# Kernel tuning notes

Measured on AMD Instinct MI355X. Metric: run time of the kernel, lower is better.

The kernel has to match this reference:

```python
import jax, jax.numpy as jnp
import numpy as np

B, HW, ENC, E, D, A, V, L = 64, 14, 2048, 512, 512, 512, 32000, 32
LN_EPS = 1e-5


def setup_inputs() -> dict:
    key = jax.random.key(0)
    ks = jax.random.split(key, 16)
    s = 0.02
    n = lambda k, sh: jax.random.normal(k, sh, jnp.float32)
    encoder_out = n(ks[0], (B, HW, HW, ENC))
    encoded_captions = jax.random.randint(ks[1], (B, L), 0, V)
    caption_lengths = jax.random.randint(ks[2], (B, 1), 2, L + 1)
    caption_lengths = caption_lengths.at[0, 0].set(L)  # ensure max length present
    return dict(
        encoder_out=encoder_out,
        encoded_captions=encoded_captions,
        caption_lengths=caption_lengths,
        emb=n(ks[3], (V, E)) * s,
        W_enc_att=n(ks[4], (A, ENC)) * s, b_enc_att=jnp.zeros((A,)),
        W_dec_att=n(ks[5], (A, D)) * s, b_dec_att=jnp.zeros((A,)),
        W_full_att=n(ks[6], (1, A)) * s, b_full_att=jnp.zeros((1,)),
        W_ih=n(ks[7], (4 * D, E + ENC)) * s, b_ih=jnp.zeros((4 * D,)),
        W_hh=n(ks[8], (4 * D, D)) * s, b_hh=jnp.zeros((4 * D,)),
        g_h=jnp.ones((D,)), be_h=jnp.zeros((D,)),
        g_c=jnp.ones((D,)), be_c=jnp.zeros((D,)),
        W_init_h=n(ks[9], (D, ENC)) * s, b_init_h=jnp.zeros((D,)),
        W_init_c=n(ks[10], (D, ENC)) * s, b_init_c=jnp.zeros((D,)),
        W_beta=n(ks[11], (ENC, D)) * s, b_beta=jnp.zeros((ENC,)),
        W_fc=n(ks[12], (V, D)) * s, b_fc=jnp.zeros((V,)),
    )


def _layer_norm(x, g, b):
    m = x.mean(-1, keepdims=True)
    v = ((x - m) ** 2).mean(-1, keepdims=True)
    return (x - m) / jnp.sqrt(v + LN_EPS) * g + b


def reference(encoder_out, encoded_captions, caption_lengths, emb,
              W_enc_att, b_enc_att, W_dec_att, b_dec_att, W_full_att, b_full_att,
              W_ih, b_ih, W_hh, b_hh, g_h, be_h, g_c, be_c,
              W_init_h, b_init_h, W_init_c, b_init_c, W_beta, b_beta, W_fc, b_fc):
    bsz = encoder_out.shape[0]
    enc_out = encoder_out.reshape(bsz, -1, encoder_out.shape[-1])  # [B,P,ENC]
    lengths = caption_lengths[:, 0]
    order = jnp.argsort(-lengths)  # stable descending sort (matches torch sort)
    lengths = lengths[order]
    enc_out = enc_out[order]
    caps = encoded_captions[order]
    embeds = emb[caps]  # [B,L,E]
    decode_lengths = lengths - 1
    T = caps.shape[1] - 1  # static max(decode_lengths)

    mean_enc = enc_out.mean(axis=1)
    h = _layer_norm(mean_enc @ W_init_h.T + b_init_h, g_h, be_h)
    c = _layer_norm(mean_enc @ W_init_c.T + b_init_c, g_c, be_c)

    att1 = enc_out @ W_enc_att.T + b_enc_att  # [B,P,A] precomputed once
    prev_seq = jnp.swapaxes(embeds[:, :T], 0, 1)  # [T,B,E] teacher-forced inputs
    masks = jnp.arange(T)[:, None] < decode_lengths[None, :]  # [T,B] active rows

    def step(carry, xs):
        h, c = carry
        prev, mask = xs
        # attention
        att2 = h @ W_dec_att.T + b_dec_att  # [B,A]
        e = jax.nn.relu(att1 + att2[:, None, :]) @ W_full_att[0] + b_full_att[0]  # [B,P]
        alpha = jax.nn.softmax(e, axis=1)
        awe = jnp.einsum('bpe,bp->be', enc_out, alpha)  # [B,ENC]
        gate = jax.nn.sigmoid(h @ W_beta.T + b_beta)
        awe = gate * awe
        # LSTM cell
        x = jnp.concatenate([prev, awe], axis=1)  # [B,E+ENC]
        gates = x @ W_ih.T + b_ih + h @ W_hh.T + b_hh
        i, f, g, o = jnp.split(gates, 4, axis=1)
        c_new = jax.nn.sigmoid(f) * c + jax.nn.sigmoid(i) * jnp.tanh(g)
        h_new = jax.nn.sigmoid(o) * jnp.tanh(c_new)
        h_new = _layer_norm(h_new, g_h, be_h)
        c_new = _layer_norm(c_new, g_c, be_c)
        preds = h_new @ W_fc.T + b_fc  # [B,V]; dropout is identity in eval
        m = mask[:, None]
        h = jnp.where(m, h_new, h)  # freeze finished rows (== torch batch shrink)
        c = jnp.where(m, c_new, c)
        return (h, c), (jnp.where(m, preds, 0.0), jnp.where(m, alpha, 0.0))

    (_, _), (preds_t, alphas_t) = jax.lax.scan(step, (h, c), (prev_seq, masks))
    predictions = jnp.swapaxes(preds_t, 0, 1)  # [B,T,V]
    alphas = jnp.swapaxes(alphas_t, 0, 1)      # [B,T,P]
    return predictions, caps, decode_lengths, alphas, order
```

## Files before the change

### kernel.cpp

```cpp
#include <hip/hip_runtime.h>
#include <cfloat>
#include <math.h>

#define B_ 64
#define P_ 196
#define ENC_ 2048
#define D_ 512
#define V_ 32000
#define L_ 32
#define T_ 31

#define OUT_PREDS 0L
#define OUT_CAPS  63488000L
#define OUT_DECL  63490048L
#define OUT_ALPH  63490112L
#define OUT_ORDER 63878976L

typedef __bf16 bf16;
typedef __bf16 bf16x8 __attribute__((ext_vector_type(8)));
typedef __bf16 bf16x4 __attribute__((ext_vector_type(4)));
typedef __bf16 bf16x2 __attribute__((ext_vector_type(2)));
typedef float  f32x4  __attribute__((ext_vector_type(4)));

static __device__ __forceinline__ float sigmoidf_(float x) { return 1.f / (1.f + __expf(-x)); }

__global__ void k_order(const int* __restrict__ cap_len, const int* __restrict__ caps,
                        int* __restrict__ order_i, int* __restrict__ declen_i,
                        int* __restrict__ caps_i, float* __restrict__ out,
                        int* __restrict__ rmap, int* __restrict__ orow, int* __restrict__ mact)
{
    __shared__ int len_s[B_], dl_s[B_];
    __shared__ int Msh;
    int tid = threadIdx.x;
    len_s[tid] = cap_len[tid];
    __syncthreads();
    int li = len_s[tid];
    int pos = 0;
    for (int j = 0; j < B_; ++j) {
        int lj = len_s[j];
        pos += (lj > li) || (lj == li && j < tid);
    }
    order_i[pos]  = tid;
    declen_i[pos] = li - 1;
    dl_s[pos]     = li - 1;
    out[OUT_ORDER + pos] = (float)tid;
    out[OUT_DECL  + pos] = (float)(li - 1);
    for (int l = 0; l < L_; ++l) {
        int tok = caps[tid * L_ + l];
        caps_i[pos * L_ + l] = tok;
        out[OUT_CAPS + pos * L_ + l] = (float)tok;
    }
    __syncthreads();
    int p = tid;
    int off = 0;
    for (int j = 0; j < p; ++j) off += dl_s[j];
    int dl = dl_s[p];
    if (p == B_ - 1) { Msh = off + dl; mact[0] = off + dl; }
    __syncthreads();
    for (int tt = 0; tt < dl; ++tt) {
        rmap[off + tt] = tt * B_ + p;
        orow[off + tt] = p * T_ + tt;
    }
    int ibase = Msh + p * T_ - off;
    for (int tt = dl; tt < T_; ++tt) {
        rmap[ibase + (tt - dl)] = 0;
        orow[ibase + (tt - dl)] = -(p * T_ + tt) - 1;
    }
}

struct CvtSegs { const float* s[3]; bf16* d[3]; long cum[4]; };
__global__ __launch_bounds__(256) void k_cvt_all(CvtSegs cs)
{
    long i8 = ((long)blockIdx.x * 256 + threadIdx.x) * 8;
    if (i8 >= cs.cum[3]) return;
    int k = 0;
    while (i8 >= cs.cum[k + 1]) ++k;
    long loc = i8 - cs.cum[k];
    const float* src = cs.s[k] + loc;
    float4 a = *(const float4*)(src);
    float4 b = *(const float4*)(src + 4);
    bf16x8 v;
    v[0]=(bf16)a.x; v[1]=(bf16)a.y; v[2]=(bf16)a.z; v[3]=(bf16)a.w;
    v[4]=(bf16)b.x; v[5]=(bf16)b.y; v[6]=(bf16)b.z; v[7]=(bf16)b.w;
    *(bf16x8*)(cs.d[k] + loc) = v;
}

template<int MODE>
__global__ __launch_bounds__(256)
void k_packB(const float* __restrict__ s1, const float* __restrict__ s2,
             bf16* __restrict__ dst, int Kv, int Nsp, int Ksp)
{
    const int ntile = blockIdx.x, tid = threadIdx.x;
    long tbase = (long)ntile * Kv * 16;
    const int groups = Kv * 2;
    for (int g = tid; g < groups; g += 256) {
        int kkq = g >> 4, r16 = g & 15;
        int n = ntile * 16 + r16, k0 = kkq * 8;
        const float* src;
        if (MODE == 0)      src = s1 + (long)n * Kv + k0;
        else if (MODE == 1) src = (n < Nsp) ? s1 + (long)n * Kv + k0
                                            : s2 + (long)(n - Nsp) * Kv + k0;
        else                src = (k0 < Ksp) ? s1 + (long)n * Ksp + k0
                                             : s2 + (long)n * (Kv - Ksp) + (k0 - Ksp);
        float4 a = *(const float4*)src;
        float4 b = *(const float4*)(src + 4);
        bf16x8 v;
        v[0]=(bf16)a.x; v[1]=(bf16)a.y; v[2]=(bf16)a.z; v[3]=(bf16)a.w;
        v[4]=(bf16)b.x; v[5]=(bf16)b.y; v[6]=(bf16)b.z; v[7]=(bf16)b.w;
        *(bf16x8*)(dst + tbase + (long)kkq * 128 + r16 * 8) = v;
    }
}

__global__ __launch_bounds__(256)
void k_packA(const bf16* __restrict__ hseq, const int* __restrict__ rmap, bf16* __restrict__ dst)
{
    const int mt = blockIdx.x, tid = threadIdx.x;
    long tbase = (long)mt * 32768;
    for (int g = tid; g < 4096; g += 256) {
        int mi = g >> 10, rem = g & 1023, kkq = rem >> 4, r16 = rem & 15;
        int row = rmap[mt * 64 + mi * 16 + r16];
        bf16x8 v = *(const bf16x8*)(hseq + (long)row * 512 + kkq * 8);
        *(bf16x8*)(dst + tbase + mi * 8192 + (long)kkq * 128 + r16 * 8) = v;
    }
}

__global__ __launch_bounds__(256) void k_cvt_enc(const float* __restrict__ enc,
                                                 const int* __restrict__ order_i,
                                                 bf16* __restrict__ enc_s)
{
    long i = ((long)blockIdx.x * 256 + threadIdx.x) * 8;
    int b = (int)(i / ((long)P_ * ENC_));
    long rem = i - (long)b * P_ * ENC_;
    const float* src = enc + (long)order_i[b] * P_ * ENC_ + rem;
    float4 a = *(const float4*)(src);
    float4 c = *(const float4*)(src + 4);
    bf16x8 v;
    v[0]=(bf16)a.x; v[1]=(bf16)a.y; v[2]=(bf16)a.z; v[3]=(bf16)a.w;
    v[4]=(bf16)c.x; v[5]=(bf16)c.y; v[6]=(bf16)c.z; v[7]=(bf16)c.w;
    *(bf16x8*)(enc_s + i) = v;
}

__global__ __launch_bounds__(256) void k_meanb(const bf16* __restrict__ enc_s, bf16* __restrict__ mean_b)
{
    int b = blockIdx.x, col = blockIdx.y * 256 + threadIdx.x;
    float s = 0.f;
    const bf16* eb = enc_s + (long)b * P_ * ENC_ + col;
    for (int p = 0; p < P_; ++p) s += (float)eb[(long)p * ENC_];
    mean_b[(long)b * ENC_ + col] = (bf16)(s * (1.f / (float)P_));
}

template<int MI, int FUSE, int EPI, int SWZ, int PK>
__global__ void __launch_bounds__(256)
k_mgemm(const bf16* __restrict__ A, long lda,
        const bf16* __restrict__ B1, const bf16* __restrict__ B2,
        const float* __restrict__ bias,
        float* __restrict__ Cf, bf16* __restrict__ Cb,
        int N, int K, int kspl, int Nsp, int Mtot)
{
    const int tid = threadIdx.x;
    const int lane = tid & 63, w = tid >> 6;
    int mt, nt, z;
    if (SWZ == 0) { mt = blockIdx.x; nt = blockIdx.y; z = blockIdx.z; }
    else          { int o = blockIdx.x; int wg = (o & 7) * 49 + (o >> 3);
                    mt = wg >> 2; nt = wg & 3; z = 0; }
    const int krange = K / kspl;
    const int k0 = z * krange, k1 = k0 + krange;
    const int r16 = lane & 15, kq = lane >> 4;
    const int koff = kq * 8;

    const bf16* Ap = A + (long)(mt * (MI * 16) + r16) * lda + koff;
    const int ncol0 = nt * 128 + w * 32;

    const bf16* Bp[2];
#pragma unroll
    for (int ni = 0; ni < 2; ++ni) {
        if (PK) {
            Bp[ni] = B1 + (long)((ncol0 + ni * 16) >> 4) * ((long)K * 16) + kq * 128 + r16 * 8;
        } else {
            int n = ncol0 + ni * 16 + r16;
            if (FUSE == 1)
                Bp[ni] = (n < Nsp) ? B1 + (long)n * K + koff
                                   : B2 + (long)(n - Nsp) * K + koff;
            else
                Bp[ni] = B1 + (long)n * K + koff;
        }
    }

    auto loadA = [&](int kk, bf16x8* dst) {
#pragma unroll
        for (int mi = 0; mi < MI; ++mi)
            dst[mi] = *(const bf16x8*)(Ap + (long)mi * 16 * lda + kk);
    };
    auto loadB = [&](int kk, bf16x8* dst) {
#pragma unroll
        for (int ni = 0; ni < 2; ++ni)
            dst[ni] = PK ? *(const bf16x8*)(Bp[ni] + (long)kk * 16)
                         : *(const bf16x8*)(Bp[ni] + kk);
    };

    f32x4 acc[MI][2] = {};
    bf16x8 af[MI], bfr[2];
    loadA(k0, af); loadB(k0, bfr);
    for (int kk = k0 + 32; kk < k1; kk += 32) {
        bf16x8 af2[MI], bf2[2];
        loadA(kk, af2); loadB(kk, bf2);
#pragma unroll
        for (int mi = 0; mi < MI; ++mi)
#pragma unroll
            for (int ni = 0; ni < 2; ++ni)
                acc[mi][ni] = __builtin_amdgcn_mfma_f32_16x16x32_bf16(bfr[ni], af[mi], acc[mi][ni], 0, 0, 0);
#pragma unroll
        for (int mi = 0; mi < MI; ++mi) af[mi] = af2[mi];
#pragma unroll
        for (int ni = 0; ni < 2; ++ni) bfr[ni] = bf2[ni];
    }
#pragma unroll
    for (int mi = 0; mi < MI; ++mi)
#pragma unroll
        for (int ni = 0; ni < 2; ++ni)
            acc[mi][ni] = __builtin_amdgcn_mfma_f32_16x16x32_bf16(bfr[ni], af[mi], acc[mi][ni], 0, 0, 0);

#pragma unroll
    for (int mi = 0; mi < MI; ++mi) {
        const int row = mt * (MI * 16) + mi * 16 + r16;
#pragma unroll
        for (int ni = 0; ni < 2; ++ni) {
            const int col = ncol0 + ni * 16 + kq * 4;
            f32x4 v = acc[mi][ni];
            if (EPI == 0) {
                *(f32x4*)(Cf + (long)z * Mtot * N + (long)row * N + col) = v;
            } else {
                f32x4 bv = *(const f32x4*)(bias + col);
                bf16x4 o;
                o[0]=(bf16)(v[0]+bv[0]); o[1]=(bf16)(v[1]+bv[1]);
                o[2]=(bf16)(v[2]+bv[2]); o[3]=(bf16)(v[3]+bv[3]);
                *(bf16x4*)(Cb + (long)row * N + col) = o;
            }
        }
    }
}

__global__ __launch_bounds__(512)
void k_initln(const float* __restrict__ pi,
              const float* __restrict__ b_h, const float* __restrict__ b_c,
              const float* __restrict__ g_h, const float* __restrict__ be_h,
              const float* __restrict__ g_c, const float* __restrict__ be_c,
              bf16* __restrict__ xh, float* __restrict__ cbuf)
{
    int b = blockIdx.x, d = threadIdx.x;
    float yh = pi[(long)b * 1024 + d]       + b_h[d];
    float yc = pi[(long)b * 1024 + 512 + d] + b_c[d];
    __shared__ float r1[512], r2[512], r3[512], r4[512];
    r1[d] = yh; r2[d] = yh * yh; r3[d] = yc; r4[d] = yc * yc;
    __syncthreads();
    for (int s = 256; s > 0; s >>= 1) {
        if (d < s) { r1[d]+=r1[d+s]; r2[d]+=r2[d+s]; r3[d]+=r3[d+s]; r4[d]+=r4[d+s]; }
        __syncthreads();
    }
    float mh = r1[0] * (1.f/512.f), vh = r2[0] * (1.f/512.f) - mh*mh;
    float mc = r3[0] * (1.f/512.f), vc = r4[0] * (1.f/512.f) - mc*mc;
    float hln = (yh - mh) * rsqrtf(vh + 1e-5f) * g_h[d] + be_h[d];
    float cln = (yc - mc) * rsqrtf(vc + 1e-5f) * g_c[d] + be_c[d];
    xh[(long)b * 3072 + 2560 + d] = (bf16)hln;
    cbuf[(long)b * 512 + d] = cln;
}

__global__ __launch_bounds__(512)
void k_attn(const float* __restrict__ att2gate, const float* __restrict__ b_dec,
            const float* __restrict__ b_beta, const float* __restrict__ Wfull,
            const bf16* __restrict__ att1_b, const bf16* __restrict__ enc_s,
            const int* __restrict__ caps_i, const int* __restrict__ declen_i,
            const float* __restrict__ emb,
            bf16* __restrict__ xh, float* __restrict__ out, int t)
{
    const int b = blockIdx.x >> 1, seg = blockIdx.x & 1, tid = threadIdx.x;
    if (t >= declen_i[b]) {
        if (seg == 1 && tid < P_) out[OUT_ALPH + ((long)b * T_ + t) * P_ + tid] = 0.f;
        return;
    }
    __shared__ float att2s[512], wf[512], red[512], alp[P_];
    {
        float s = b_dec[tid];
#pragma unroll
        for (int zz = 0; zz < 4; ++zz) s += att2gate[((long)zz * 64 + b) * 2560 + tid];
        att2s[tid] = s;
        wf[tid] = Wfull[tid];
    }
    __syncthreads();
    float ev = -FLT_MAX;
    if (tid < P_) {
        const bf16* ar = att1_b + ((long)b * P_ + tid) * 512;
        float acc = 0.f;
        for (int a0 = 0; a0 < 512; a0 += 8) {
            bf16x8 v = *(const bf16x8*)(ar + a0);
#pragma unroll
            for (int j = 0; j < 8; ++j)
                acc += fmaxf((float)v[j] + att2s[a0 + j], 0.f) * wf[a0 + j];
        }
        ev = acc;
    }
    red[tid] = ev;
    __syncthreads();
    for (int s = 256; s > 0; s >>= 1) { if (tid < s) red[tid] = fmaxf(red[tid], red[tid + s]); __syncthreads(); }
    float mx = red[0];
    __syncthreads();
    float ex = (tid < P_) ? __expf(ev - mx) : 0.f;
    red[tid] = ex;
    __syncthreads();
    for (int s = 256; s > 0; s >>= 1) { if (tid < s) red[tid] += red[tid + s]; __syncthreads(); }
    float inv = 1.f / red[0];
    if (tid < P_) alp[tid] = ex * inv;
    __syncthreads();
    if (seg == 1 && tid < P_)
        out[OUT_ALPH + ((long)b * T_ + t) * P_ + tid] = alp[tid];
    const int c0 = seg * 1024 + tid * 2;
    const bf16* eb = enc_s + (long)b * P_ * ENC_ + c0;
    float a0 = 0.f, a1 = 0.f;
#pragma unroll 4
    for (int p = 0; p < P_; ++p) {
        bf16x2 v = *(const bf16x2*)(eb + (long)p * ENC_);
        float al = alp[p];
        a0 += al * (float)v[0]; a1 += al * (float)v[1];
    }
    float g0 = b_beta[c0], g1 = b_beta[c0 + 1];
#pragma unroll
    for (int zz = 0; zz < 4; ++zz) {
        const float* gs = att2gate + ((long)zz * 64 + b) * 2560 + 512 + c0;
        g0 += gs[0]; g1 += gs[1];
    }
    bf16x2 o;
    o[0] = (bf16)(a0 * sigmoidf_(g0));
    o[1] = (bf16)(a1 * sigmoidf_(g1));
    *(bf16x2*)(xh + (long)b * 3072 + 512 + c0) = o;
    if (seg == 0) {
        int tok = caps_i[b * L_ + t];
        xh[(long)b * 3072 + tid] = (bf16)emb[(long)tok * 512 + tid];
    }
}

__global__ __launch_bounds__(512)
void k_lstm(const float* __restrict__ gp, const float* __restrict__ b_ih, const float* __restrict__ b_hh,
            const float* __restrict__ g_h, const float* __restrict__ be_h,
            const float* __restrict__ g_c, const float* __restrict__ be_c,
            bf16* __restrict__ xh, float* __restrict__ cbuf, bf16* __restrict__ hseq,
            const int* __restrict__ declen_i, int t)
{
    int b = blockIdx.x, d = threadIdx.x;
    if (t >= declen_i[b]) return;
    float iv = b_ih[d]        + b_hh[d];
    float fv = b_ih[512 + d]  + b_hh[512 + d];
    float gv = b_ih[1024 + d] + b_hh[1024 + d];
    float ov = b_ih[1536 + d] + b_hh[1536 + d];
#pragma unroll
    for (int s = 0; s < 8; ++s) {
        const float* gs = gp + ((long)s * B_ + b) * 2048;
        iv += gs[d]; fv += gs[512 + d]; gv += gs[1024 + d]; ov += gs[1536 + d];
    }
    float cn = sigmoidf_(fv) * cbuf[(long)b * 512 + d] + sigmoidf_(iv) * tanhf(gv);
    float hn = sigmoidf_(ov) * tanhf(cn);
    __shared__ float r1[512], r2[512], r3[512], r4[512];
    r1[d] = hn; r2[d] = hn * hn; r3[d] = cn; r4[d] = cn * cn;
    __syncthreads();
    for (int s = 256; s > 0; s >>= 1) {
        if (d < s) { r1[d]+=r1[d+s]; r2[d]+=r2[d+s]; r3[d]+=r3[d+s]; r4[d]+=r4[d+s]; }
        __syncthreads();
    }
    float mh = r1[0] * (1.f/512.f), vh = r2[0] * (1.f/512.f) - mh*mh;
    float mc = r3[0] * (1.f/512.f), vc = r4[0] * (1.f/512.f) - mc*mc;
    float hln = (hn - mh) * rsqrtf(vh + 1e-5f) * g_h[d] + be_h[d];
    float cln = (cn - mc) * rsqrtf(vc + 1e-5f) * g_c[d] + be_c[d];
    bf16 hv = (bf16)hln;
    xh[(long)b * 3072 + 2560 + d] = hv;
    hseq[((long)t * B_ + b) * 512 + d] = hv;
    cbuf[(long)b * 512 + d] = cln;
}

__global__ __launch_bounds__(256)
void k_preds(const bf16* __restrict__ Apk, const bf16* __restrict__ Bpk,
             const float* __restrict__ bias, const int* __restrict__ orow,
             const int* __restrict__ mact, float* __restrict__ out)
{
    int o = blockIdx.x; int xcd = o & 7;
    int base = xcd < 6 ? xcd * 969 : 5814 + (xcd - 6) * 968;
    int wg = base + (o >> 3);
    int nt = wg / 31, mt = wg - 31 * nt;
    __shared__ int os[64];
    __shared__ __align__(16) float ct[64][132];
    const int tid = threadIdx.x, lane = tid & 63, w = tid >> 6;
    const int r16 = lane & 15, kq = lane >> 4;
    if (tid < 64) os[tid] = orow[mt * 64 + tid];
    __syncthreads();
    const int r0 = tid >> 5, cc = (tid & 31) * 4;
    const int gcol = nt * 128 + cc;
    if (mt * 64 >= mact[0]) {
        f32x4 zz = {0.f, 0.f, 0.f, 0.f};
#pragma unroll
        for (int it = 0; it < 8; ++it) {
            int r = it * 8 + r0;
            int row = -os[r] - 1;
            *(f32x4*)(out + OUT_PREDS + (long)row * V_ + gcol) = zz;
        }
        return;
    }
    const bf16* Ap[4];
#pragma unroll
    for (int mi = 0; mi < 4; ++mi)
        Ap[mi] = Apk + (long)mt * 32768 + mi * 8192 + kq * 128 + r16 * 8;
    const bf16* Bp[2];
#pragma unroll
    for (int ni = 0; ni < 2; ++ni)
        Bp[ni] = Bpk + (long)((nt * 128 + w * 32 + ni * 16) >> 4) * 8192 + kq * 128 + r16 * 8;

    f32x4 acc[4][2] = {};
    bf16x8 af[4], bfr[2];
#pragma unroll
    for (int mi = 0; mi < 4; ++mi) af[mi] = *(const bf16x8*)(Ap[mi]);
#pragma unroll
    for (int ni = 0; ni < 2; ++ni) bfr[ni] = *(const bf16x8*)(Bp[ni]);
    for (int kk = 32; kk < 512; kk += 32) {
        bf16x8 af2[4], bf2[2];
#pragma unroll
        for (int mi = 0; mi < 4; ++mi) af2[mi] = *(const bf16x8*)(Ap[mi] + kk * 16);
#pragma unroll
        for (int ni = 0; ni < 2; ++ni) bf2[ni] = *(const bf16x8*)(Bp[ni] + kk * 16);
#pragma unroll
        for (int mi = 0; mi < 4; ++mi)
#pragma unroll
            for (int ni = 0; ni < 2; ++ni)
                acc[mi][ni] = __builtin_amdgcn_mfma_f32_16x16x32_bf16(bfr[ni], af[mi], acc[mi][ni], 0, 0, 0);
#pragma unroll
        for (int mi = 0; mi < 4; ++mi) af[mi] = af2[mi];
#pragma unroll
        for (int ni = 0; ni < 2; ++ni) bfr[ni] = bf2[ni];
    }
#pragma unroll
    for (int mi = 0; mi < 4; ++mi)
#pragma unroll
        for (int ni = 0; ni < 2; ++ni)
            acc[mi][ni] = __builtin_amdgcn_mfma_f32_16x16x32_bf16(bfr[ni], af[mi], acc[mi][ni], 0, 0, 0);

#pragma unroll
    for (int mi = 0; mi < 4; ++mi)
#pragma unroll
        for (int ni = 0; ni < 2; ++ni)
            *(f32x4*)&ct[mi * 16 + r16][w * 32 + ni * 16 + kq * 4] = acc[mi][ni];
    __syncthreads();
    f32x4 bv = *(const f32x4*)(bias + gcol);
    f32x4 zz = {0.f, 0.f, 0.f, 0.f};
#pragma unroll
    for (int it = 0; it < 8; ++it) {
        int r = it * 8 + r0;
        int orv = os[r];
        if (orv >= 0) {
            f32x4 v = *(f32x4*)&ct[r][cc];
            f32x4 oo;
            oo[0] = v[0] + bv[0]; oo[1] = v[1] + bv[1];
            oo[2] = v[2] + bv[2]; oo[3] = v[3] + bv[3];
            *(f32x4*)(out + OUT_PREDS + (long)orv * V_ + gcol) = oo;
        } else {
            int row = -orv - 1;
            *(f32x4*)(out + OUT_PREDS + (long)row * V_ + gcol) = zz;
        }
    }
}

extern "C" void kernel_launch(void* const* d_in, const int* in_sizes, int n_in,
                              void* d_out, int out_size, void* d_ws, size_t ws_size,
                              hipStream_t stream)
{
    const float* enc       = (const float*)d_in[0];
    const int*   caps      = (const int*)  d_in[1];
    const int*   caplen    = (const int*)  d_in[2];
    const float* emb       = (const float*)d_in[3];
    const float* W_enc_att = (const float*)d_in[4];
    const float* b_enc_att = (const float*)d_in[5];
    const float* W_dec_att = (const float*)d_in[6];
    const float* b_dec_att = (const float*)d_in[7];
    const float* W_full    = (const float*)d_in[8];
    const float* W_ih      = (const float*)d_in[10];
    const float* b_ih      = (const float*)d_in[11];
    const float* W_hh      = (const float*)d_in[12];
    const float* b_hh      = (const float*)d_in[13];
    const float* g_h       = (const float*)d_in[14];
    const float* be_h      = (const float*)d_in[15];
    const float* g_c       = (const float*)d_in[16];
    const float* be_c      = (const float*)d_in[17];
    const float* W_init_h  = (const float*)d_in[18];
    const float* b_init_h  = (const float*)d_in[19];
    const float* W_init_c  = (const float*)d_in[20];
    const float* b_init_c  = (const float*)d_in[21];
    const float* W_beta    = (const float*)d_in[22];
    const float* b_beta    = (const float*)d_in[23];
    const float* W_fc      = (const float*)d_in[24];
    const float* b_fc      = (const float*)d_in[25];
    float* out = (float*)d_out;

    char* w = (char*)d_ws;
    auto alloc = [&](size_t bytes) { char* p = w; w += (bytes + 255) & ~(size_t)255; return p; };
    int*   order_i  = (int*)  alloc(B_ * 4);
    int*   declen_i = (int*)  alloc(B_ * 4);
    int*   caps_i   = (int*)  alloc(B_ * L_ * 4);
    int*   rmap     = (int*)  alloc(2048 * 4);
    int*   orow     = (int*)  alloc(2048 * 4);
    int*   mact     = (int*)  alloc(256);
    bf16*  enc_s    = (bf16*) alloc((size_t)B_ * P_ * ENC_ * 2);
    bf16*  mean_b   = (bf16*) alloc((size_t)B_ * ENC_ * 2);
    bf16*  att1_b   = (bf16*) alloc((size_t)B_ * P_ * 512 * 2);
    float* pi       = (float*)alloc((size_t)B_ * 1024 * 4);
    float* cbuf     = (float*)alloc((size_t)B_ * 512 * 4);
    bf16*  xh       = (bf16*) alloc((size_t)B_ * 3072 * 2);
    float* att2gate = (float*)alloc((size_t)4 * B_ * 2560 * 4);
    float* gp       = (float*)alloc((size_t)8 * B_ * 2048 * 4);
    bf16*  hseq     = (bf16*) alloc((size_t)T_ * B_ * 512 * 2);
    bf16*  Apk      = (bf16*) alloc((size_t)31 * 32768 * 2);
    bf16*  W_enc_b  = (bf16*) alloc((size_t)512 * 2048 * 2);
    bf16*  W_inh_b  = (bf16*) alloc((size_t)512 * 2048 * 2);
    bf16*  W_inc_b  = (bf16*) alloc((size_t)512 * 2048 * 2);
    bf16*  Wab_pk   = (bf16*) alloc((size_t)2560 * 512 * 2);
    bf16*  Wg_pk    = (bf16*) alloc((size_t)2048 * 3072 * 2);
    bf16*  Wfc_pk   = (bf16*) alloc((size_t)32000 * 512 * 2);

    k_order<<<1, B_, 0, stream>>>(caplen, caps, order_i, declen_i, caps_i, out, rmap, orow, mact);
    k_cvt_enc<<<12544, 256, 0, stream>>>(enc, order_i, enc_s);
    k_meanb<<<dim3(B_, 8), 256, 0, stream>>>(enc_s, mean_b);

    CvtSegs cs;
    const float* srcs[3] = {W_enc_att, W_init_h, W_init_c};
    bf16* dsts[3] = {W_enc_b, W_inh_b, W_inc_b};
    long ns[3] = {512L*2048, 512L*2048, 512L*2048};
    long cum = 0;
    for (int i = 0; i < 3; ++i) { cs.s[i] = srcs[i]; cs.d[i] = dsts[i]; cs.cum[i] = cum; cum += ns[i]; }
    cs.cum[3] = cum;
    k_cvt_all<<<(int)((cum / 8 + 255) / 256), 256, 0, stream>>>(cs);

    k_packB<1><<<160, 256, 0, stream>>>(W_dec_att, W_beta, Wab_pk, 512, 512, 0);
    k_packB<2><<<128, 256, 0, stream>>>(W_ih, W_hh, Wg_pk, 3072, 0, 2560);
    k_packB<0><<<2000, 256, 0, stream>>>(W_fc, nullptr, Wfc_pk, 512, 0, 0);

    k_mgemm<4, 1, 0, 0, 0><<<dim3(1, 8, 1), 256, 0, stream>>>(mean_b, 2048, W_inh_b, W_inc_b,
        nullptr, pi, nullptr, 1024, 2048, 1, 512, 64);
    k_initln<<<B_, 512, 0, stream>>>(pi, b_init_h, b_init_c, g_h, be_h, g_c, be_c, xh, cbuf);

    k_mgemm<8, 0, 1, 1, 0><<<392, 256, 0, stream>>>(enc_s, 2048, W_enc_b, nullptr,
        b_enc_att, nullptr, att1_b, 512, 2048, 1, 0, 12544);

    for (int t = 0; t < T_; ++t) {
        k_mgemm<4, 0, 0, 0, 1><<<dim3(1, 20, 4), 256, 0, stream>>>(xh + 2560, 3072, Wab_pk, nullptr,
            nullptr, att2gate, nullptr, 2560, 512, 4, 0, 64);
        k_attn<<<128, 512, 0, stream>>>(att2gate, b_dec_att, b_beta, W_full, att1_b, enc_s,
            caps_i, declen_i, emb, xh, out, t);
        k_mgemm<4, 0, 0, 0, 1><<<dim3(1, 16, 8), 256, 0, stream>>>(xh, 3072, Wg_pk, nullptr,
            nullptr, gp, nullptr, 2048, 3072, 8, 0, 64);
        k_lstm<<<B_, 512, 0, stream>>>(gp, b_ih, b_hh, g_h, be_h, g_c, be_c,
            xh, cbuf, hseq, declen_i, t);
    }

    k_packA<<<31, 256, 0, stream>>>(hseq, rmap, Apk);
    k_preds<<<7750, 256, 0, stream>>>(Apk, Wfc_pk, b_fc, orow, mact, out);
}
```

Baseline: 2.086 ms.

## Pack encoder activations and W_enc_att into MFMA tile layout for att1 GEMM

```diff
diff --git a/kernel.cpp b/kernel.cpp
--- a/kernel.cpp
+++ b/kernel.cpp
@@ -68,11 +68,11 @@
     }
 }
 
-struct CvtSegs { const float* s[3]; bf16* d[3]; long cum[4]; };
+struct CvtSegs { const float* s[2]; bf16* d[2]; long cum[3]; };
 __global__ __launch_bounds__(256) void k_cvt_all(CvtSegs cs)
 {
     long i8 = ((long)blockIdx.x * 256 + threadIdx.x) * 8;
-    if (i8 >= cs.cum[3]) return;
+    if (i8 >= cs.cum[2]) return;
     int k = 0;
     while (i8 >= cs.cum[k + 1]) ++k;
     long loc = i8 - cs.cum[k];
@@ -126,9 +126,12 @@
 
 __global__ __launch_bounds__(256) void k_cvt_enc(const float* __restrict__ enc,
                                                  const int* __restrict__ order_i,
-                                                 bf16* __restrict__ enc_s)
+                                                 bf16* __restrict__ enc_s,
+                                                 bf16* __restrict__ enc_pk)
 {
     long i = ((long)blockIdx.x * 256 + threadIdx.x) * 8;
+    int r = (int)(i >> 11);
+    int k0 = (int)(i & 2047);
     int b = (int)(i / ((long)P_ * ENC_));
     long rem = i - (long)b * P_ * ENC_;
     const float* src = enc + (long)order_i[b] * P_ * ENC_ + rem;
@@ -138,6 +141,7 @@
     v[0]=(bf16)a.x; v[1]=(bf16)a.y; v[2]=(bf16)a.z; v[3]=(bf16)a.w;
     v[4]=(bf16)c.x; v[5]=(bf16)c.y; v[6]=(bf16)c.z; v[7]=(bf16)c.w;
     *(bf16x8*)(enc_s + i) = v;
+    *(bf16x8*)(enc_pk + (long)(r >> 4) * 32768 + (long)(k0 >> 3) * 128 + (r & 15) * 8) = v;
 }
 
 __global__ __launch_bounds__(256) void k_meanb(const bf16* __restrict__ enc_s, bf16* __restrict__ mean_b)
@@ -149,7 +153,7 @@
     mean_b[(long)b * ENC_ + col] = (bf16)(s * (1.f / (float)P_));
 }
 
-template<int MI, int FUSE, int EPI, int SWZ, int PK>
+template<int MI, int FUSE, int EPI, int SWZ, int PK, int PA>
 __global__ void __launch_bounds__(256)
 k_mgemm(const bf16* __restrict__ A, long lda,
         const bf16* __restrict__ B1, const bf16* __restrict__ B2,
@@ -161,14 +165,19 @@
     const int lane = tid & 63, w = tid >> 6;
     int mt, nt, z;
     if (SWZ == 0) { mt = blockIdx.x; nt = blockIdx.y; z = blockIdx.z; }
-    else          { int o = blockIdx.x; int wg = (o & 7) * 49 + (o >> 3);
+    else          { int o = blockIdx.x; int wg = (o & 7) * 98 + (o >> 3);
                     mt = wg >> 2; nt = wg & 3; z = 0; }
     const int krange = K / kspl;
     const int k0 = z * krange, k1 = k0 + krange;
     const int r16 = lane & 15, kq = lane >> 4;
     const int koff = kq * 8;
 
-    const bf16* Ap = A + (long)(mt * (MI * 16) + r16) * lda + koff;
+    const bf16* Ap[MI];
+#pragma unroll
+    for (int mi = 0; mi < MI; ++mi) {
+        if (PA) Ap[mi] = A + (long)(mt * MI + mi) * ((long)K * 16) + kq * 128 + r16 * 8;
+        else    Ap[mi] = A + (long)(mt * (MI * 16) + mi * 16 + r16) * lda + koff;
+    }
     const int ncol0 = nt * 128 + w * 32;
 
     const bf16* Bp[2];
@@ -189,7 +198,8 @@
     auto loadA = [&](int kk, bf16x8* dst) {
 #pragma unroll
         for (int mi = 0; mi < MI; ++mi)
-            dst[mi] = *(const bf16x8*)(Ap + (long)mi * 16 * lda + kk);
+            dst[mi] = PA ? *(const bf16x8*)(Ap[mi] + (long)kk * 16)
+                         : *(const bf16x8*)(Ap[mi] + kk);
     };
     auto loadB = [&](int kk, bf16x8* dst) {
 #pragma unroll
@@ -504,6 +514,7 @@
     int*   orow     = (int*)  alloc(2048 * 4);
     int*   mact     = (int*)  alloc(256);
     bf16*  enc_s    = (bf16*) alloc((size_t)B_ * P_ * ENC_ * 2);
+    bf16*  enc_pk   = (bf16*) alloc((size_t)B_ * P_ * ENC_ * 2);
     bf16*  mean_b   = (bf16*) alloc((size_t)B_ * ENC_ * 2);
     bf16*  att1_b   = (bf16*) alloc((size_t)B_ * P_ * 512 * 2);
     float* pi       = (float*)alloc((size_t)B_ * 1024 * 4);
@@ -513,43 +524,44 @@
     float* gp       = (float*)alloc((size_t)8 * B_ * 2048 * 4);
     bf16*  hseq     = (bf16*) alloc((size_t)T_ * B_ * 512 * 2);
     bf16*  Apk      = (bf16*) alloc((size_t)31 * 32768 * 2);
-    bf16*  W_enc_b  = (bf16*) alloc((size_t)512 * 2048 * 2);
     bf16*  W_inh_b  = (bf16*) alloc((size_t)512 * 2048 * 2);
     bf16*  W_inc_b  = (bf16*) alloc((size_t)512 * 2048 * 2);
+    bf16*  Wenc_pk  = (bf16*) alloc((size_t)512 * 2048 * 2);
     bf16*  Wab_pk   = (bf16*) alloc((size_t)2560 * 512 * 2);
     bf16*  Wg_pk    = (bf16*) alloc((size_t)2048 * 3072 * 2);
     bf16*  Wfc_pk   = (bf16*) alloc((size_t)32000 * 512 * 2);
 
     k_order<<<1, B_, 0, stream>>>(caplen, caps, order_i, declen_i, caps_i, out, rmap, orow, mact);
-    k_cvt_enc<<<12544, 256, 0, stream>>>(enc, order_i, enc_s);
+    k_cvt_enc<<<12544, 256, 0, stream>>>(enc, order_i, enc_s, enc_pk);
     k_meanb<<<dim3(B_, 8), 256, 0, stream>>>(enc_s, mean_b);
 
     CvtSegs cs;
-    const float* srcs[3] = {W_enc_att, W_init_h, W_init_c};
-    bf16* dsts[3] = {W_enc_b, W_inh_b, W_inc_b};
-    long ns[3] = {512L*2048, 512L*2048, 512L*2048};
+    const float* srcs[2] = {W_init_h, W_init_c};
+    bf16* dsts[2] = {W_inh_b, W_inc_b};
+    long ns[2] = {512L*2048, 512L*2048};
     long cum = 0;
-    for (int i = 0; i < 3; ++i) { cs.s[i] = srcs[i]; cs.d[i] = dsts[i]; cs.cum[i] = cum; cum += ns[i]; }
-    cs.cum[3] = cum;
+    for (int i = 0; i < 2; ++i) { cs.s[i] = srcs[i]; cs.d[i] = dsts[i]; cs.cum[i] = cum; cum += ns[i]; }
+    cs.cum[2] = cum;
     k_cvt_all<<<(int)((cum / 8 + 255) / 256), 256, 0, stream>>>(cs);
 
+    k_packB<0><<<32, 256, 0, stream>>>(W_enc_att, nullptr, Wenc_pk, 2048, 0, 0);
     k_packB<1><<<160, 256, 0, stream>>>(W_dec_att, W_beta, Wab_pk, 512, 512, 0);
     k_packB<2><<<128, 256, 0, stream>>>(W_ih, W_hh, Wg_pk, 3072, 0, 2560);
     k_packB<0><<<2000, 256, 0, stream>>>(W_fc, nullptr, Wfc_pk, 512, 0, 0);
 
-    k_mgemm<4, 1, 0, 0, 0><<<dim3(1, 8, 1), 256, 0, stream>>>(mean_b, 2048, W_inh_b, W_inc_b,
+    k_mgemm<4, 1, 0, 0, 0, 0><<<dim3(1, 8, 1), 256, 0, stream>>>(mean_b, 2048, W_inh_b, W_inc_b,
         nullptr, pi, nullptr, 1024, 2048, 1, 512, 64);
     k_initln<<<B_, 512, 0, stream>>>(pi, b_init_h, b_init_c, g_h, be_h, g_c, be_c, xh, cbuf);
 
-    k_mgemm<8, 0, 1, 1, 0><<<392, 256, 0, stream>>>(enc_s, 2048, W_enc_b, nullptr,
+    k_mgemm<4, 0, 1, 1, 1, 1><<<784, 256, 0, stream>>>(enc_pk, 0, Wenc_pk, nullptr,
         b_enc_att, nullptr, att1_b, 512, 2048, 1, 0, 12544);
 
     for (int t = 0; t < T_; ++t) {
-        k_mgemm<4, 0, 0, 0, 1><<<dim3(1, 20, 4), 256, 0, stream>>>(xh + 2560, 3072, Wab_pk, nullptr,
+        k_mgemm<4, 0, 0, 0, 1, 0><<<dim3(1, 20, 4), 256, 0, stream>>>(xh + 2560, 3072, Wab_pk, nullptr,
             nullptr, att2gate, nullptr, 2560, 512, 4, 0, 64);
         k_attn<<<128, 512, 0, stream>>>(att2gate, b_dec_att, b_beta, W_full, att1_b, enc_s,
             caps_i, declen_i, emb, xh, out, t);
-        k_mgemm<4, 0, 0, 0, 1><<<dim3(1, 16, 8), 256, 0, stream>>>(xh, 3072, Wg_pk, nullptr,
+        k_mgemm<4, 0, 0, 0, 1, 0><<<dim3(1, 16, 8), 256, 0, stream>>>(xh, 3072, Wg_pk, nullptr,
             nullptr, gp, nullptr, 2048, 3072, 8, 0, 64);
         k_lstm<<<B_, 512, 0, stream>>>(gp, b_ih, b_hh, g_h, be_h, g_c, be_c,
             xh, cbuf, hseq, declen_i, t);
```

Result: no change. 2.086 ms (median of 2 runs) (+0.0%).
